# Kernel optimization log

Measured on AMD Instinct MI355X. Metric: run time of the kernel, lower is better.

Reference implementation:

```python
import jax, jax.numpy as jnp
import numpy as np

B, D, H, L = 8, 512, 512, 8192


def _log_g(x):
    # log_g(x) = log(relu(x)+1) if x>=0 else x
    return jnp.where(x >= 0, jnp.log1p(jax.nn.relu(x)), x)


def setup_inputs() -> dict:
    key = jax.random.key(0)
    k1, k2, k3 = jax.random.split(key, 3)
    x = jax.random.normal(k1, (B, D, L), dtype=jnp.float32)
    # Conv1d(dim, 2*h_dim, kernel_size=1) weight [2H, D, 1] squeezed to [2H, D]
    W = jax.random.normal(k2, (2 * H, D), dtype=jnp.float32) / np.sqrt(D).astype(np.float32)
    b = jax.random.normal(k3, (2 * H,), dtype=jnp.float32) * 0.02
    return {"x": x, "W": W, "b": b}


def reference(x, W, b):
    # 1x1 conv == pointwise linear over channels: [B, 2H, L]
    hg = jnp.einsum('od,bdl->bol', W, x) + b[None, :, None]
    h, gate = jnp.split(hg, 2, axis=1)  # each [B, H, L]
    log_coeffs = -jax.nn.softplus(gate)                 # log(1 - sigmoid(gate))
    log_values = -jax.nn.softplus(-gate) + _log_g(h)    # log(sigmoid(gate)) + log_g(h)
    a_star = jnp.cumsum(log_coeffs, axis=2)
    log_h = a_star + jax.lax.cumlogsumexp(log_values - a_star, axis=2)
    return jnp.exp(log_h)  # [B, H, L]
```

## Files before the change

kernel.cpp:

```cpp
#include <hip/hip_runtime.h>
#include <hip/hip_fp16.h>

#define B_  8
#define D_  512
#define H_  512
#define L_  8192
#define O2_ 1024

typedef __attribute__((ext_vector_type(8))) short   bf16x8;
typedef __attribute__((ext_vector_type(4))) float   floatx4;
typedef __attribute__((ext_vector_type(8))) unsigned short ushort8_t;
typedef __attribute__((ext_vector_type(4))) unsigned short ushort4_t;

__device__ __forceinline__ unsigned short f2bf(float f) {
    union { float f; unsigned u; } x; x.f = f;
    unsigned u = x.u;
    u += 0x7FFFu + ((u >> 16) & 1u);
    return (unsigned short)(u >> 16);
}

__global__ __launch_bounds__(256) void prep_w(const float* __restrict__ W,
                                              unsigned short* __restrict__ Wr) {
    int idx  = blockIdx.x * 256 + threadIdx.x;
    int flat = idx * 4;
    int o = flat >> 9;
    int d = flat & 511;
    int src_o = (o & 1) ? (H_ + (o >> 1)) : (o >> 1);
    float4 wv = *(const float4*)(W + (size_t)src_o * D_ + d);
    ushort4_t r;
    r.x = f2bf(wv.x); r.y = f2bf(wv.y); r.z = f2bf(wv.z); r.w = f2bf(wv.w);
    *(ushort4_t*)(Wr + (size_t)o * D_ + d) = r;
}

__global__ __launch_bounds__(256) void transpose_x(const float* __restrict__ x,
                                                   unsigned short* __restrict__ xT) {
    __shared__ float T[64][65];
    const int b  = blockIdx.z;
    const int d0 = blockIdx.y * 64;
    const int l0 = blockIdx.x * 64;
    const int tid = threadIdx.x;

    const int c  = tid & 15;
    const int r0 = tid >> 4;
    const float* xp = x + ((size_t)b * D_ + d0) * L_ + l0;
    for (int rr = r0; rr < 64; rr += 16) {
        float4 vv = *(const float4*)(xp + (size_t)rr * L_ + c * 4);
        T[c * 4 + 0][rr] = vv.x;
        T[c * 4 + 1][rr] = vv.y;
        T[c * 4 + 2][rr] = vv.z;
        T[c * 4 + 3][rr] = vv.w;
    }
    __syncthreads();

    const int dc  = (tid & 7) * 8;
    const int lr0 = tid >> 3;
    unsigned short* op = xT + ((size_t)b * L_ + l0) * D_ + d0;
    for (int lr = lr0; lr < 64; lr += 32) {
        ushort8_t o8;
        o8[0] = f2bf(T[lr][dc + 0]); o8[1] = f2bf(T[lr][dc + 1]);
        o8[2] = f2bf(T[lr][dc + 2]); o8[3] = f2bf(T[lr][dc + 3]);
        o8[4] = f2bf(T[lr][dc + 4]); o8[5] = f2bf(T[lr][dc + 5]);
        o8[6] = f2bf(T[lr][dc + 6]); o8[7] = f2bf(T[lr][dc + 7]);
        *(ushort8_t*)(op + (size_t)lr * D_ + dc) = o8;
    }
}

__global__ __launch_bounds__(256) void gemm_hg(const unsigned short* __restrict__ Wr,
                                               const unsigned short* __restrict__ xT,
                                               __half* __restrict__ hg) {
    __shared__ unsigned short As[128][72];
    __shared__ unsigned short Bs[128][72];

    const int b  = blockIdx.z;
    const int o0 = blockIdx.y * 128;
    const int l0 = blockIdx.x * 128;
    const int tid  = threadIdx.x;
    const int lane = tid & 63;
    const int w    = tid >> 6;
    const int wm   = (w >> 1) * 64;
    const int wn   = (w & 1) * 64;
    const int lm   = lane & 15;
    const int quad = lane >> 4;

    floatx4 acc[4][4];
    for (int mi = 0; mi < 4; ++mi)
        for (int ni = 0; ni < 4; ++ni)
            acc[mi][ni] = (floatx4){0.f, 0.f, 0.f, 0.f};

    const int srow = tid >> 3;
    const int scol = (tid & 7) * 8;
    const unsigned short* Ab = Wr + (size_t)(o0 + srow) * D_ + scol;
    const unsigned short* Bb = xT + ((size_t)b * L_ + l0 + srow) * D_ + scol;

    for (int kk = 0; kk < 8; ++kk) {
        const int k0 = kk * 64;
        for (int p = 0; p < 4; ++p) {
            uint4 av = *(const uint4*)(Ab + (size_t)(p * 32) * D_ + k0);
            uint4 bv = *(const uint4*)(Bb + (size_t)(p * 32) * D_ + k0);
            *(uint4*)&As[srow + p * 32][scol] = av;
            *(uint4*)&Bs[srow + p * 32][scol] = bv;
        }
        __syncthreads();

        for (int ks = 0; ks < 2; ++ks) {
            const int koff = ks * 32 + quad * 8;
            bf16x8 af[4], bfv[4];
            for (int mi = 0; mi < 4; ++mi)
                af[mi] = *(const bf16x8*)&As[wm + mi * 16 + lm][koff];
            for (int ni = 0; ni < 4; ++ni)
                bfv[ni] = *(const bf16x8*)&Bs[wn + ni * 16 + lm][koff];
            for (int mi = 0; mi < 4; ++mi)
                for (int ni = 0; ni < 4; ++ni)
                    acc[mi][ni] = __builtin_amdgcn_mfma_f32_16x16x32_bf16(
                        af[mi], bfv[ni], acc[mi][ni], 0, 0, 0);
        }
        __syncthreads();
    }

    __half* hp = hg + ((size_t)b * O2_ + o0 + wm + quad * 4) * L_ + l0 + wn + lm;
    for (int mi = 0; mi < 4; ++mi)
        for (int ni = 0; ni < 4; ++ni)
            for (int r = 0; r < 4; ++r)
                hp[(size_t)(mi * 16 + r) * L_ + ni * 16] = __float2half(acc[mi][ni][r]);
}

__global__ __launch_bounds__(256) void scan_seq(const __half* __restrict__ hg,
                                                const float* __restrict__ bias,
                                                float* __restrict__ out) {
    __shared__ float sA[256];
    __shared__ float sB[256];
    const int bid = blockIdx.x;
    const int b = bid >> 9;
    const int k = bid & 511;
    const int t = threadIdx.x;

    const __half* hp = hg + ((size_t)b * O2_ + 2 * k) * L_ + t * 32;
    const __half* gp = hp + L_;
    const float bh = bias[k];
    const float bg = bias[H_ + k];

    union U { uint4 q; __half h[8]; };
    U hu[4], gu[4];
    const uint4* hq = (const uint4*)hp;
    const uint4* gq = (const uint4*)gp;
    for (int i = 0; i < 4; ++i) { hu[i].q = hq[i]; gu[i].q = gq[i]; }

    float c[32], v[32];
    float A = 1.f, Bv = 0.f;
    for (int i = 0; i < 32; ++i) {
        float hf = __half2float(hu[i >> 3].h[i & 7]) + bh;
        float gf = __half2float(gu[i >> 3].h[i & 7]) + bg;
        float e   = __expf(gf);
        float inv = 1.f / (1.f + e);
        float ci  = inv;
        float zi  = e * inv;
        float gv  = (hf >= 0.f) ? (1.f + hf) : __expf(hf);
        float vi  = zi * gv;
        c[i] = ci; v[i] = vi;
        Bv = ci * Bv + vi;
        A *= ci;
    }

    sA[t] = A; sB[t] = Bv;
    __syncthreads();
    for (int off = 1; off < 256; off <<= 1) {
        float pA = 1.f, pB = 0.f;
        if (t >= off) { pA = sA[t - off]; pB = sB[t - off]; }
        __syncthreads();
        Bv = Bv + A * pB;
        A  = A * pA;
        sA[t] = A; sB[t] = Bv;
        __syncthreads();
    }
    float hr = (t > 0) ? sB[t - 1] : 0.f;

    float* op = out + ((size_t)b * H_ + k) * L_ + t * 32;
    for (int i = 0; i < 32; i += 4) {
        float4 o4;
        o4.x = hr = c[i + 0] * hr + v[i + 0];
        o4.y = hr = c[i + 1] * hr + v[i + 1];
        o4.z = hr = c[i + 2] * hr + v[i + 2];
        o4.w = hr = c[i + 3] * hr + v[i + 3];
        *(float4*)(op + i) = o4;
    }
}

__global__ __launch_bounds__(256) void fused_naive(const float* __restrict__ x,
                                                   const float* __restrict__ W,
                                                   const float* __restrict__ bias,
                                                   float* __restrict__ out) {
    __shared__ float Wh[512];
    __shared__ float Wg[512];
    __shared__ float sA[256];
    __shared__ float sB[256];
    const int bid = blockIdx.x;
    const int b = bid >> 9;
    const int k = bid & 511;
    const int t = threadIdx.x;

    for (int i = t; i < 512; i += 256) {
        Wh[i] = W[(size_t)k * D_ + i];
        Wg[i] = W[(size_t)(H_ + k) * D_ + i];
    }
    const float bh = bias[k];
    const float bg = bias[H_ + k];
    __syncthreads();

    float Hc = 0.f;
    const float* xb = x + (size_t)b * D_ * L_;
    for (int ch = 0; ch < 32; ++ch) {
        const int l = ch * 256 + t;
        float ah = bh, ag = bg;
        for (int d = 0; d < 512; ++d) {
            float xv = xb[(size_t)d * L_ + l];
            ah += Wh[d] * xv;
            ag += Wg[d] * xv;
        }
        float e   = __expf(ag);
        float inv = 1.f / (1.f + e);
        float ci  = inv;
        float zi  = e * inv;
        float gv  = (ah >= 0.f) ? (1.f + ah) : __expf(ah);
        float vi  = zi * gv;

        float A = ci, Bv = vi;
        sA[t] = A; sB[t] = Bv;
        __syncthreads();
        for (int off = 1; off < 256; off <<= 1) {
            float pA = 1.f, pB = 0.f;
            if (t >= off) { pA = sA[t - off]; pB = sB[t - off]; }
            __syncthreads();
            Bv = Bv + A * pB;
            A  = A * pA;
            sA[t] = A; sB[t] = Bv;
            __syncthreads();
        }
        out[((size_t)b * H_ + k) * L_ + l] = A * Hc + Bv;
        float An = sA[255], Bn = sB[255];
        Hc = An * Hc + Bn;
        __syncthreads();
    }
}

extern "C" void kernel_launch(void* const* d_in, const int* in_sizes, int n_in,
                              void* d_out, int out_size, void* d_ws, size_t ws_size,
                              hipStream_t stream) {
    const float* x    = (const float*)d_in[0];
    const float* W    = (const float*)d_in[1];
    const float* bias = (const float*)d_in[2];
    float* out = (float*)d_out;

    const size_t xT_bytes = (size_t)B_ * L_ * D_ * 2;
    const size_t Wr_bytes = (size_t)O2_ * D_ * 2;
    const size_t hg_bytes = (size_t)B_ * O2_ * L_ * 2;
    const size_t need = xT_bytes + Wr_bytes + hg_bytes;

    if (ws_size >= need) {
        char* ws = (char*)d_ws;
        unsigned short* xT = (unsigned short*)ws;
        unsigned short* Wr = (unsigned short*)(ws + xT_bytes);
        __half*         hg = (__half*)(ws + xT_bytes + Wr_bytes);

        prep_w<<<512, 256, 0, stream>>>(W, Wr);
        transpose_x<<<dim3(L_ / 64, D_ / 64, B_), 256, 0, stream>>>(x, xT);
        gemm_hg<<<dim3(L_ / 128, O2_ / 128, B_), 256, 0, stream>>>(Wr, xT, hg);
        scan_seq<<<B_ * H_, 256, 0, stream>>>(hg, bias, out);
    } else {
        fused_naive<<<B_ * H_, 256, 0, stream>>>(x, W, bias, out);
    }
}
```

Baseline: 367.9 us.

## Use async global-to-LDS loads in GEMM and stage scan I/O through LDS

The GEMM tile loads now use global_load_lds to copy data straight into unpadded shared memory, skipping the register round trip, and the inner loops are fully unrolled. The scan kernel now stages its fp16 inputs and fp32 outputs through padded shared memory, so global reads and writes are coalesced across threads instead of each thread touching its own 64-byte or 128-byte strided chunk. Dropping the GEMM padding may add LDS bank conflicts. The larger shared buffer in the scan kernel, with a 3-blocks occupancy hint, costs occupancy.

```diff
diff --git a/kernel.cpp b/kernel.cpp
--- a/kernel.cpp
+++ b/kernel.cpp
@@ -17,6 +17,13 @@
     unsigned u = x.u;
     u += 0x7FFFu + ((u >> 16) & 1u);
     return (unsigned short)(u >> 16);
+}
+
+__device__ __forceinline__ void async_load16(const void* g, void* l) {
+    __builtin_amdgcn_global_load_lds(
+        (const __attribute__((address_space(1))) unsigned int*)g,
+        (__attribute__((address_space(3))) unsigned int*)l,
+        16, 0, 0);
 }
 
 __global__ __launch_bounds__(256) void prep_w(const float* __restrict__ W,
@@ -68,8 +75,8 @@
 __global__ __launch_bounds__(256) void gemm_hg(const unsigned short* __restrict__ Wr,
                                                const unsigned short* __restrict__ xT,
                                                __half* __restrict__ hg) {
-    __shared__ unsigned short As[128][72];
-    __shared__ unsigned short Bs[128][72];
+    __shared__ __align__(16) unsigned short As[128][64];
+    __shared__ __align__(16) unsigned short Bs[128][64];
 
     const int b  = blockIdx.z;
     const int o0 = blockIdx.y * 128;
@@ -87,29 +94,33 @@
         for (int ni = 0; ni < 4; ++ni)
             acc[mi][ni] = (floatx4){0.f, 0.f, 0.f, 0.f};
 
-    const int srow = tid >> 3;
-    const int scol = (tid & 7) * 8;
-    const unsigned short* Ab = Wr + (size_t)(o0 + srow) * D_ + scol;
-    const unsigned short* Bb = xT + ((size_t)b * L_ + l0 + srow) * D_ + scol;
+    const int srow = w * 32 + (lane >> 3);
+    const int scol = (lane & 7) * 8;
+    const unsigned short* Ag = Wr + (size_t)(o0 + srow) * D_ + scol;
+    const unsigned short* Bg = xT + ((size_t)b * L_ + l0 + srow) * D_ + scol;
 
     for (int kk = 0; kk < 8; ++kk) {
         const int k0 = kk * 64;
+        #pragma unroll
         for (int p = 0; p < 4; ++p) {
-            uint4 av = *(const uint4*)(Ab + (size_t)(p * 32) * D_ + k0);
-            uint4 bv = *(const uint4*)(Bb + (size_t)(p * 32) * D_ + k0);
-            *(uint4*)&As[srow + p * 32][scol] = av;
-            *(uint4*)&Bs[srow + p * 32][scol] = bv;
-        }
-        __syncthreads();
-
+            async_load16(Ag + (size_t)(p * 8) * D_ + k0, &As[w * 32 + p * 8][0]);
+            async_load16(Bg + (size_t)(p * 8) * D_ + k0, &Bs[w * 32 + p * 8][0]);
+        }
+        __syncthreads();
+
+        #pragma unroll
         for (int ks = 0; ks < 2; ++ks) {
             const int koff = ks * 32 + quad * 8;
             bf16x8 af[4], bfv[4];
+            #pragma unroll
             for (int mi = 0; mi < 4; ++mi)
                 af[mi] = *(const bf16x8*)&As[wm + mi * 16 + lm][koff];
+            #pragma unroll
             for (int ni = 0; ni < 4; ++ni)
                 bfv[ni] = *(const bf16x8*)&Bs[wn + ni * 16 + lm][koff];
+            #pragma unroll
             for (int mi = 0; mi < 4; ++mi)
+                #pragma unroll
                 for (int ni = 0; ni < 4; ++ni)
                     acc[mi][ni] = __builtin_amdgcn_mfma_f32_16x16x32_bf16(
                         af[mi], bfv[ni], acc[mi][ni], 0, 0, 0);
@@ -124,41 +135,64 @@
                 hp[(size_t)(mi * 16 + r) * L_ + ni * 16] = __float2half(acc[mi][ni][r]);
 }
 
-__global__ __launch_bounds__(256) void scan_seq(const __half* __restrict__ hg,
-                                                const float* __restrict__ bias,
-                                                float* __restrict__ out) {
+__global__ __launch_bounds__(256, 3) void scan_seq(const __half* __restrict__ hg,
+                                                   const float* __restrict__ bias,
+                                                   float* __restrict__ out) {
+    __shared__ __align__(16) unsigned int sBuf[256 * 40];
     __shared__ float sA[256];
     __shared__ float sB[256];
+    unsigned int* sH = sBuf;
+    unsigned int* sG = sBuf + 256 * 20;
+
     const int bid = blockIdx.x;
     const int b = bid >> 9;
     const int k = bid & 511;
     const int t = threadIdx.x;
 
-    const __half* hp = hg + ((size_t)b * O2_ + 2 * k) * L_ + t * 32;
-    const __half* gp = hp + L_;
+    const uint4* hq = (const uint4*)(hg + ((size_t)b * O2_ + 2 * k) * L_);
+    const uint4* gq = hq + (L_ / 8);
+
+    #pragma unroll
+    for (int j = 0; j < 4; ++j) {
+        int idx = t + 256 * j;
+        uint4 hv = hq[idx];
+        uint4 gv = gq[idx];
+        int cc = idx >> 2, ss = idx & 3;
+        *(uint4*)&sH[cc * 20 + ss * 4] = hv;
+        *(uint4*)&sG[cc * 20 + ss * 4] = gv;
+    }
     const float bh = bias[k];
     const float bg = bias[H_ + k];
-
-    union U { uint4 q; __half h[8]; };
-    U hu[4], gu[4];
-    const uint4* hq = (const uint4*)hp;
-    const uint4* gq = (const uint4*)gp;
-    for (int i = 0; i < 4; ++i) { hu[i].q = hq[i]; gu[i].q = gq[i]; }
+    __syncthreads();
 
     float c[32], v[32];
     float A = 1.f, Bv = 0.f;
-    for (int i = 0; i < 32; ++i) {
-        float hf = __half2float(hu[i >> 3].h[i & 7]) + bh;
-        float gf = __half2float(gu[i >> 3].h[i & 7]) + bg;
-        float e   = __expf(gf);
-        float inv = 1.f / (1.f + e);
-        float ci  = inv;
-        float zi  = e * inv;
-        float gv  = (hf >= 0.f) ? (1.f + hf) : __expf(hf);
-        float vi  = zi * gv;
-        c[i] = ci; v[i] = vi;
-        Bv = ci * Bv + vi;
-        A *= ci;
+    #pragma unroll
+    for (int j4 = 0; j4 < 4; ++j4) {
+        uint4 hv = *(const uint4*)&sH[t * 20 + j4 * 4];
+        uint4 gv = *(const uint4*)&sG[t * 20 + j4 * 4];
+        unsigned hu[4] = {hv.x, hv.y, hv.z, hv.w};
+        unsigned gu[4] = {gv.x, gv.y, gv.z, gv.w};
+        #pragma unroll
+        for (int q = 0; q < 4; ++q) {
+            __half2 h2 = *(const __half2*)&hu[q];
+            __half2 g2 = *(const __half2*)&gu[q];
+            #pragma unroll
+            for (int e = 0; e < 2; ++e) {
+                const int i = j4 * 8 + q * 2 + e;
+                float hf = (e ? __high2float(h2) : __low2float(h2)) + bh;
+                float gf = (e ? __high2float(g2) : __low2float(g2)) + bg;
+                float ex  = __expf(gf);
+                float inv = 1.f / (1.f + ex);
+                float ci  = inv;
+                float zi  = ex * inv;
+                float gv2 = (hf >= 0.f) ? (1.f + hf) : __expf(hf);
+                float vi  = zi * gv2;
+                c[i] = ci; v[i] = vi;
+                Bv = ci * Bv + vi;
+                A *= ci;
+            }
+        }
     }
 
     sA[t] = A; sB[t] = Bv;
@@ -174,14 +208,24 @@
     }
     float hr = (t > 0) ? sB[t - 1] : 0.f;
 
-    float* op = out + ((size_t)b * H_ + k) * L_ + t * 32;
+    float* sO = (float*)sBuf;
+    #pragma unroll
     for (int i = 0; i < 32; i += 4) {
         float4 o4;
         o4.x = hr = c[i + 0] * hr + v[i + 0];
         o4.y = hr = c[i + 1] * hr + v[i + 1];
         o4.z = hr = c[i + 2] * hr + v[i + 2];
         o4.w = hr = c[i + 3] * hr + v[i + 3];
-        *(float4*)(op + i) = o4;
+        *(float4*)&sO[t * 36 + i] = o4;
+    }
+    __syncthreads();
+
+    float4* op4 = (float4*)(out + ((size_t)b * H_ + k) * L_);
+    #pragma unroll
+    for (int j = 0; j < 8; ++j) {
+        int idx = t + 256 * j;
+        int cc = idx >> 3, ss = idx & 7;
+        op4[idx] = *(const float4*)&sO[cc * 36 + ss * 4];
     }
 }
 
```

Result: no change. 362.3 us (-1.5%).
